# Kernel optimization log

Measured on AMD Instinct MI355X. Metric: run time of the kernel, lower is better.

The kernel has to match this reference:

```python
import jax, jax.numpy as jnp
import numpy as np

B, L = 128, 1024
V, E, H = 32, 256, 1024


def setup_inputs() -> dict:
    key = jax.random.key(0)
    ks = jax.random.split(key, 6)
    return {
        "x": jax.random.randint(ks[0], (B, L), 0, V),
        "hidden": jnp.zeros((B, H), dtype=jnp.float32),
        "embedding": jax.random.normal(ks[1], (V, E), dtype=jnp.float32),
        "W_e": jax.random.normal(ks[2], (E, H), dtype=jnp.float32) * 0.01,
        "W_h": jax.random.normal(ks[3], (H, H), dtype=jnp.float32) * 0.01,
        "b_h": jnp.zeros((H,), dtype=jnp.float32),
        "W_o": jax.random.normal(ks[4], (H, V), dtype=jnp.float32) * 0.01,
        "b_o": jnp.zeros((V,), dtype=jnp.float32),
    }


def reference(x, hidden, embedding, W_e, W_h, b_h, W_o, b_o):
    # x: [B, L] int -> embed: [B, L, E]
    x_embed = embedding[x]
    # Precompute the input projection for all timesteps at once: [L, B, H]
    xin = jnp.einsum("ble,eh->lbh", x_embed, W_e) + b_h

    def step(h, x_t):
        # h: [B, H], x_t: [B, H] (already projected + bias)
        h_new = jnp.tanh(x_t + h @ W_h)
        return h_new, h_new

    final_hidden, outputs = jax.lax.scan(step, hidden, xin)
    # outputs: [L, B, H] -> [B, L, H]
    outputs = outputs.transpose(1, 0, 2)
    logits = outputs @ W_o + b_o  # [B, L, V]
    return logits, final_hidden
```

## Files before the change

### kernel.cpp

```cpp
#include <hip/hip_runtime.h>

typedef unsigned short u16;
typedef unsigned int   u32;
typedef __attribute__((ext_vector_type(4))) float floatx4;
typedef __attribute__((ext_vector_type(4))) u32  u32x4;
typedef __attribute__((ext_vector_type(8))) short short8;

#define B_SZ  128
#define L_SEQ 1024
#define V_SZ  32
#define E_SZ  256
#define H_SZ  1024

#define N_GROUPS     8
#define WG_PER_GROUP 8
#define N_BLOCKS     (N_GROUPS * WG_PER_GROUP)
#define LOGIT_BASE   (B_SZ * L_SEQ * V_SZ)

#define BAR_BYTES  8192
#define FLAG_OFF   (BAR_BYTES - 8)
#define P_OFF      BAR_BYTES
#define P_BYTES    (V_SZ * H_SZ * 4)
#define HBUF_OFF   (P_OFF + P_BYTES)
#define NBUF       4
#define HBUF_G     (NBUF * 16 * H_SZ)
#define HBUF_BYTES (N_GROUPS * HBUF_G * 2)

#define SENT 0xFFFFFFFFu

#define MFMA16x16x32(a, b, c) __builtin_amdgcn_mfma_f32_16x16x32_bf16(a, b, c, 0, 0, 0)

__device__ inline float b2f(u16 u) {
    union { unsigned i; float f; } x; x.i = ((unsigned)u) << 16; return x.f;
}
__device__ inline u16 f2b(float f) {
    unsigned u = __float_as_uint(f);
    return (u16)((u + 0x7FFFu + ((u >> 16) & 1u)) >> 16);
}
__device__ inline float ldf(const void* p, long i, int isf32) {
    return isf32 ? ((const float*)p)[i] : b2f(((const u16*)p)[i]);
}
__device__ inline u16 ldb(const void* p, long i, int isf32) {
    return isf32 ? f2b(((const float*)p)[i]) : ((const u16*)p)[i];
}

__device__ inline void ld_row16_raw(const u16* abase, u32x4 a[8]) {
    u32x4 a0, a1, a2, a3, a4, a5, a6, a7;
    asm volatile(
        "global_load_dwordx4 %0, %8, off offset:0   sc0 sc1\n\t"
        "global_load_dwordx4 %1, %8, off offset:64  sc0 sc1\n\t"
        "global_load_dwordx4 %2, %8, off offset:128 sc0 sc1\n\t"
        "global_load_dwordx4 %3, %8, off offset:192 sc0 sc1\n\t"
        "global_load_dwordx4 %4, %8, off offset:256 sc0 sc1\n\t"
        "global_load_dwordx4 %5, %8, off offset:320 sc0 sc1\n\t"
        "global_load_dwordx4 %6, %8, off offset:384 sc0 sc1\n\t"
        "global_load_dwordx4 %7, %8, off offset:448 sc0 sc1\n\t"
        "s_waitcnt vmcnt(0)"
        : "=&v"(a0), "=&v"(a1), "=&v"(a2), "=&v"(a3),
          "=&v"(a4), "=&v"(a5), "=&v"(a6), "=&v"(a7)
        : "v"(abase)
        : "memory");
    a[0] = a0; a[1] = a1; a[2] = a2; a[3] = a3;
    a[4] = a4; a[5] = a5; a[6] = a6; a[7] = a7;
}
__device__ inline int row_ok(const u32x4 a[8]) {
    int ok = 1;
    #pragma unroll
    for (int j = 0; j < 8; ++j)
        #pragma unroll
        for (int d = 0; d < 4; ++d)
            ok &= (a[j][d] != SENT);
    return ok;
}
__device__ inline void poll_row16(const u16* abase, short8 afr[8]) {
    u32x4 av[8];
    ld_row16_raw(abase, av);
    long guard = 0;
    while (!__all(row_ok(av))) {
        if (++guard > 100000L) break;
        ld_row16_raw(abase, av);
    }
    union { u32x4 v; short8 s; } u;
    #pragma unroll
    for (int j = 0; j < 8; ++j) { u.v = av[j]; afr[j] = u.s; }
}
__device__ inline void st_row16(u32* p, u32x4 d) {
    asm volatile("global_store_dwordx4 %0, %1, off sc0 sc1" :: "v"(p), "v"(d) : "memory");
}

__global__ void detect_dtype(const u16* __restrict__ emb, const int* __restrict__ xi,
                             int* __restrict__ flag) {
    float v = b2f(emb[threadIdx.x]);
    if (!(fabsf(v) <= 1.0e6f)) atomicOr(flag, 1);
    if (xi[2 * threadIdx.x + 1] != 0) atomicOr(flag, 2);
}

__global__ void precompute_P(const void* __restrict__ emb, const void* __restrict__ We,
                             const void* __restrict__ bh, float* __restrict__ P,
                             const int* __restrict__ flag) {
    const int isf32 = *flag & 1;
    int o = blockIdx.x * 256 + threadIdx.x;
    int v = o >> 10, h = o & (H_SZ - 1);
    float acc = ldf(bh, h, isf32);
    for (int e = 0; e < E_SZ; ++e)
        acc += ldf(emb, v * E_SZ + e, isf32) * ldf(We, (long)e * H_SZ + h, isf32);
    P[o] = acc;
}

__global__ void __launch_bounds__(256, 1) rnn_kernel(
    const void* __restrict__ xp, const void* __restrict__ hidden,
    const void* __restrict__ Wh, const void* __restrict__ Wo,
    const void* __restrict__ bo, const float* __restrict__ P,
    u16* __restrict__ hbuf, float* __restrict__ out,
    const int* __restrict__ flag)
{
    __shared__ __align__(16) float red[12800];

    const int fl    = *flag;
    const int isf32 = fl & 1;
    const int xi64  = !(fl & 2);
    const int g     = blockIdx.x & 7;
    const int wg    = blockIdx.x >> 3;
    const int col0  = wg * 128;
    const int b0    = g * 16;
    const int tid   = threadIdx.x;
    const int wave  = tid >> 6;
    const int lane  = tid & 63;
    const int lrow  = lane & 15;
    const int quad  = lane >> 4;
    const int kwave = wave * 256;

    const int* x32       = (const int*)xp;
    const long long* x64 = (const long long*)xp;

    u16* hb = hbuf + g * HBUF_G;

    short8 whf[8][8], wof[2][8];
    #pragma unroll
    for (int kk = 0; kk < 8; ++kk) {
        const int kb = kwave + kk * 32 + quad * 8;
        #pragma unroll
        for (int j = 0; j < 8; ++j) {
            #pragma unroll
            for (int nt = 0; nt < 8; ++nt)
                whf[nt][kk][j] = (short)ldb(Wh, (long)(kb + j) * H_SZ + col0 + nt * 16 + lrow, isf32);
            wof[0][kk][j] = (short)ldb(Wo, (long)(kb + j) * V_SZ + lrow, isf32);
            wof[1][kk][j] = (short)ldb(Wo, (long)(kb + j) * V_SZ + 16 + lrow, isf32);
        }
    }

    const int bq = tid >> 4;
    const int c0 = (tid & 15) * 8;
    const float bov0 = ldf(bo, (tid & 15) * 2, isf32);
    const float bov1 = ldf(bo, (tid & 15) * 2 + 1, isf32);

    {
        u32x4 d;
        #pragma unroll
        for (int p = 0; p < 4; ++p) {
            u16 lo = ldb(hidden, (long)(b0 + bq) * H_SZ + col0 + c0 + 2 * p, isf32);
            u16 hi = ldb(hidden, (long)(b0 + bq) * H_SZ + col0 + c0 + 2 * p + 1, isf32);
            d[p] = (u32)lo | ((u32)hi << 16);
        }
        st_row16((u32*)(hb + bq * H_SZ + col0 + c0), d);
    }

    for (int s = 0; s < L_SEQ; ++s) {
        const u16* hc = hb + (s & 3) * (16 * H_SZ);
        u16* hn       = hb + ((s + 1) & 3) * (16 * H_SZ);
        u16* hcl      = hb + ((s + 3) & 3) * (16 * H_SZ);
        const bool do_logit = (wg == (s & 7));

        long xoff = (long)(b0 + bq) * L_SEQ + s;
        int xv = xi64 ? (int)x64[xoff] : x32[xoff];
        const floatx4* pp = (const floatx4*)(P + (long)xv * H_SZ + col0 + c0);
        floatx4 pv0 = pp[0], pv1 = pp[1];

        short8 afr[8];
        poll_row16(hc + lrow * H_SZ + kwave + quad * 8, afr);

        floatx4 acc[8] = {};
        #pragma unroll
        for (int kk = 0; kk < 8; ++kk)
            #pragma unroll
            for (int nt = 0; nt < 8; ++nt)
                acc[nt] = MFMA16x16x32(afr[kk], whf[nt][kk], acc[nt]);

        #pragma unroll
        for (int nt = 0; nt < 8; ++nt)
            #pragma unroll
            for (int r = 0; r < 4; ++r)
                red[wave * 2560 + nt * 320 + (quad * 4 + r) * 20 + lrow] = acc[nt][r];
        __syncthreads();

        {
            const int base = (c0 >> 4) * 320 + bq * 20 + (c0 & 15);
            floatx4 s0 = {0,0,0,0}, s1 = {0,0,0,0};
            #pragma unroll
            for (int w = 0; w < 4; ++w) {
                s0 += *(const floatx4*)&red[w * 2560 + base];
                s1 += *(const floatx4*)&red[w * 2560 + base + 4];
            }
            float h[8];
            #pragma unroll
            for (int j = 0; j < 4; ++j) h[j]     = tanhf(s0[j] + pv0[j]);
            #pragma unroll
            for (int j = 0; j < 4; ++j) h[4 + j] = tanhf(s1[j] + pv1[j]);
            u32x4 d;
            #pragma unroll
            for (int p = 0; p < 4; ++p)
                d[p] = (u32)f2b(h[2 * p]) | ((u32)f2b(h[2 * p + 1]) << 16);
            st_row16((u32*)(hn + bq * H_SZ + col0 + c0), d);
            if (s == L_SEQ - 1) {
                float* op = out + LOGIT_BASE + (long)(b0 + bq) * H_SZ + col0 + c0;
                ((floatx4*)op)[0] = floatx4{h[0], h[1], h[2], h[3]};
                ((floatx4*)op)[1] = floatx4{h[4], h[5], h[6], h[7]};
            }
        }
        {
            u32x4 f = { SENT, SENT, SENT, SENT };
            st_row16((u32*)(hcl + bq * H_SZ + col0 + c0), f);
        }
        __syncthreads();

        if (do_logit && s >= 1) {
            floatx4 aL0 = {0,0,0,0}, aL1 = {0,0,0,0};
            #pragma unroll
            for (int kk = 0; kk < 8; ++kk) {
                aL0 = MFMA16x16x32(afr[kk], wof[0][kk], aL0);
                aL1 = MFMA16x16x32(afr[kk], wof[1][kk], aL1);
            }
            #pragma unroll
            for (int r = 0; r < 4; ++r) {
                red[10240 + wave * 640 +       (quad * 4 + r) * 20 + lrow] = aL0[r];
                red[10240 + wave * 640 + 320 + (quad * 4 + r) * 20 + lrow] = aL1[r];
            }
            __syncthreads();
            int v0 = (tid & 15) * 2;
            int lb = 10240 + (v0 >> 4) * 320 + bq * 20 + (v0 & 15);
            float q0 = 0.f, q1 = 0.f;
            #pragma unroll
            for (int w = 0; w < 4; ++w) {
                q0 += red[lb + w * 640];
                q1 += red[lb + w * 640 + 1];
            }
            long ob = ((long)(b0 + bq) * L_SEQ + (s - 1)) * V_SZ + v0;
            out[ob]     = q0 + bov0;
            out[ob + 1] = q1 + bov1;
        }
    }

    if (wg == 0) {
        short8 afr[8];
        poll_row16(hb + lrow * H_SZ + kwave + quad * 8, afr);
        floatx4 aL0 = {0,0,0,0}, aL1 = {0,0,0,0};
        #pragma unroll
        for (int kk = 0; kk < 8; ++kk) {
            aL0 = MFMA16x16x32(afr[kk], wof[0][kk], aL0);
            aL1 = MFMA16x16x32(afr[kk], wof[1][kk], aL1);
        }
        #pragma unroll
        for (int r = 0; r < 4; ++r) {
            red[10240 + wave * 640 +       (quad * 4 + r) * 20 + lrow] = aL0[r];
            red[10240 + wave * 640 + 320 + (quad * 4 + r) * 20 + lrow] = aL1[r];
        }
        __syncthreads();
        {
            int v0 = (tid & 15) * 2;
            int lb = 10240 + (v0 >> 4) * 320 + bq * 20 + (v0 & 15);
            float q0 = 0.f, q1 = 0.f;
            #pragma unroll
            for (int w = 0; w < 4; ++w) {
                q0 += red[lb + w * 640];
                q1 += red[lb + w * 640 + 1];
            }
            long ob = ((long)(b0 + bq) * L_SEQ + (L_SEQ - 1)) * V_SZ + v0;
            out[ob]     = q0 + bov0;
            out[ob + 1] = q1 + bov1;
        }
    }
}

extern "C" void kernel_launch(void* const* d_in, const int* in_sizes, int n_in,
                              void* d_out, int out_size, void* d_ws, size_t ws_size,
                              hipStream_t stream) {
    (void)in_sizes; (void)n_in; (void)out_size; (void)ws_size;
    const void* x      = d_in[0];
    const void* hidden = d_in[1];
    const void* emb    = d_in[2];
    const void* We     = d_in[3];
    const void* Wh     = d_in[4];
    const void* bh     = d_in[5];
    const void* Wo     = d_in[6];
    const void* bo     = d_in[7];
    float* out = (float*)d_out;

    char* ws = (char*)d_ws;
    int*   flag = (int*)(ws + FLAG_OFF);
    float* P    = (float*)(ws + P_OFF);
    u16*   hbuf = (u16*)(ws + HBUF_OFF);

    hipMemsetAsync(ws, 0, BAR_BYTES, stream);
    hipMemsetAsync(ws + HBUF_OFF, 0xFF, HBUF_BYTES, stream);

    detect_dtype<<<dim3(1), dim3(256), 0, stream>>>((const u16*)emb, (const int*)x, flag);
    precompute_P<<<dim3(128), dim3(256), 0, stream>>>(emb, We, bh, P, flag);

    rnn_kernel<<<dim3(N_BLOCKS), dim3(256), 0, stream>>>(
        x, hidden, Wh, Wo, bo, P, hbuf, out, flag);
}
```

Before: 3.632 ms.

## Poll hidden-state chunks independently and overlap MFMAs with arrival; use fast tanh

```diff
diff --git a/kernel.cpp b/kernel.cpp
--- a/kernel.cpp
+++ b/kernel.cpp
@@ -44,45 +44,39 @@
     return isf32 ? f2b(((const float*)p)[i]) : ((const u16*)p)[i];
 }
 
-__device__ inline void ld_row16_raw(const u16* abase, u32x4 a[8]) {
-    u32x4 a0, a1, a2, a3, a4, a5, a6, a7;
-    asm volatile(
-        "global_load_dwordx4 %0, %8, off offset:0   sc0 sc1\n\t"
-        "global_load_dwordx4 %1, %8, off offset:64  sc0 sc1\n\t"
-        "global_load_dwordx4 %2, %8, off offset:128 sc0 sc1\n\t"
-        "global_load_dwordx4 %3, %8, off offset:192 sc0 sc1\n\t"
-        "global_load_dwordx4 %4, %8, off offset:256 sc0 sc1\n\t"
-        "global_load_dwordx4 %5, %8, off offset:320 sc0 sc1\n\t"
-        "global_load_dwordx4 %6, %8, off offset:384 sc0 sc1\n\t"
-        "global_load_dwordx4 %7, %8, off offset:448 sc0 sc1\n\t"
-        "s_waitcnt vmcnt(0)"
-        : "=&v"(a0), "=&v"(a1), "=&v"(a2), "=&v"(a3),
-          "=&v"(a4), "=&v"(a5), "=&v"(a6), "=&v"(a7)
-        : "v"(abase)
-        : "memory");
-    a[0] = a0; a[1] = a1; a[2] = a2; a[3] = a3;
-    a[4] = a4; a[5] = a5; a[6] = a6; a[7] = a7;
-}
-__device__ inline int row_ok(const u32x4 a[8]) {
-    int ok = 1;
-    #pragma unroll
-    for (int j = 0; j < 8; ++j)
-        #pragma unroll
-        for (int d = 0; d < 4; ++d)
-            ok &= (a[j][d] != SENT);
-    return ok;
-}
-__device__ inline void poll_row16(const u16* abase, short8 afr[8]) {
-    u32x4 av[8];
-    ld_row16_raw(abase, av);
-    long guard = 0;
-    while (!__all(row_ok(av))) {
-        if (++guard > 100000L) break;
-        ld_row16_raw(abase, av);
-    }
-    union { u32x4 v; short8 s; } u;
-    #pragma unroll
-    for (int j = 0; j < 8; ++j) { u.v = av[j]; afr[j] = u.s; }
+__device__ inline float fast_tanh(float x) {
+    float cx = fminf(fmaxf(x, -15.f), 15.f);
+    float t  = __builtin_amdgcn_exp2f(cx * 2.88539004f);
+    return (t - 1.f) * __builtin_amdgcn_rcpf(t + 1.f);
+}
+
+#define LOADC(dst, base, OFFLIT) \
+    asm volatile("global_load_dwordx4 %0, %1, off offset:" OFFLIT " sc0 sc1" \
+                 : "=&v"(dst) : "v"(base) : "memory")
+#define WAITVM0() asm volatile("s_waitcnt vmcnt(0)" ::: "memory")
+
+#define ISSUE_ALL8(av, ab) do { \
+    LOADC(av[0], ab, "0");   LOADC(av[1], ab, "64");  \
+    LOADC(av[2], ab, "128"); LOADC(av[3], ab, "192"); \
+    LOADC(av[4], ab, "256"); LOADC(av[5], ab, "320"); \
+    LOADC(av[6], ab, "384"); LOADC(av[7], ab, "448"); \
+    WAITVM0(); } while (0)
+
+#define REISSUE_STALE(av, ab, done) do { \
+    if (!((done) & 1))   LOADC(av[0], ab, "0");   \
+    if (!((done) & 2))   LOADC(av[1], ab, "64");  \
+    if (!((done) & 4))   LOADC(av[2], ab, "128"); \
+    if (!((done) & 8))   LOADC(av[3], ab, "192"); \
+    if (!((done) & 16))  LOADC(av[4], ab, "256"); \
+    if (!((done) & 32))  LOADC(av[5], ab, "320"); \
+    if (!((done) & 64))  LOADC(av[6], ab, "384"); \
+    if (!((done) & 128)) LOADC(av[7], ab, "448"); \
+    WAITVM0(); } while (0)
+
+__device__ inline u32 maxdw4(u32x4 a) {
+    u32 m0 = a[0] > a[1] ? a[0] : a[1];
+    u32 m1 = a[2] > a[3] ? a[2] : a[3];
+    return m0 > m1 ? m0 : m1;
 }
 __device__ inline void st_row16(u32* p, u32x4 d) {
     asm volatile("global_store_dwordx4 %0, %1, off sc0 sc1" :: "v"(p), "v"(d) : "memory");
@@ -176,16 +170,37 @@
         const floatx4* pp = (const floatx4*)(P + (long)xv * H_SZ + col0 + c0);
         floatx4 pv0 = pp[0], pv1 = pp[1];
 
+        const u16* ab = hc + lrow * H_SZ + kwave + quad * 8;
+        u32x4 av[8];
         short8 afr[8];
-        poll_row16(hc + lrow * H_SZ + kwave + quad * 8, afr);
-
         floatx4 acc[8] = {};
-        #pragma unroll
-        for (int kk = 0; kk < 8; ++kk)
-            #pragma unroll
-            for (int nt = 0; nt < 8; ++nt)
-                acc[nt] = MFMA16x16x32(afr[kk], whf[nt][kk], acc[nt]);
-
+        ISSUE_ALL8(av, ab);
+        int done = 0;
+        long guard = 0;
+        for (;;) {
+            int nd = done;
+            #pragma unroll
+            for (int j = 0; j < 8; ++j) {
+                if (!(done & (1 << j))) {
+                    if (__all((int)(maxdw4(av[j]) != SENT))) {
+                        nd |= (1 << j);
+                        union { u32x4 v; short8 s; } u; u.v = av[j];
+                        afr[j] = u.s;
+                        __builtin_amdgcn_s_setprio(1);
+                        #pragma unroll
+                        for (int nt = 0; nt < 8; ++nt)
+                            acc[nt] = MFMA16x16x32(afr[j], whf[nt][j], acc[nt]);
+                        __builtin_amdgcn_s_setprio(0);
+                    }
+                }
+            }
+            done = nd;
+            if (done == 255) break;
+            if (++guard > 200000L) break;
+            REISSUE_STALE(av, ab, done);
+        }
+
+        __builtin_amdgcn_s_setprio(1);
         #pragma unroll
         for (int nt = 0; nt < 8; ++nt)
             #pragma unroll
@@ -203,9 +218,9 @@
             }
             float h[8];
             #pragma unroll
-            for (int j = 0; j < 4; ++j) h[j]     = tanhf(s0[j] + pv0[j]);
-            #pragma unroll
-            for (int j = 0; j < 4; ++j) h[4 + j] = tanhf(s1[j] + pv1[j]);
+            for (int j = 0; j < 4; ++j) h[j]     = fast_tanh(s0[j] + pv0[j]);
+            #pragma unroll
+            for (int j = 0; j < 4; ++j) h[4 + j] = fast_tanh(s1[j] + pv1[j]);
             u32x4 d;
             #pragma unroll
             for (int p = 0; p < 4; ++p)
@@ -217,6 +232,7 @@
                 ((floatx4*)op)[1] = floatx4{h[4], h[5], h[6], h[7]};
             }
         }
+        __builtin_amdgcn_s_setprio(0);
         {
             u32x4 f = { SENT, SENT, SENT, SENT };
             st_row16((u32*)(hcl + bq * H_SZ + col0 + c0), f);
@@ -251,8 +267,27 @@
     }
 
     if (wg == 0) {
+        const u16* ab = hb + lrow * H_SZ + kwave + quad * 8;
+        u32x4 av[8];
+        ISSUE_ALL8(av, ab);
+        int done = 0;
+        long guard = 0;
+        for (;;) {
+            int nd = done;
+            #pragma unroll
+            for (int j = 0; j < 8; ++j)
+                if (!(done & (1 << j)))
+                    if (__all((int)(maxdw4(av[j]) != SENT))) nd |= (1 << j);
+            done = nd;
+            if (done == 255) break;
+            if (++guard > 200000L) break;
+            REISSUE_STALE(av, ab, done);
+        }
         short8 afr[8];
-        poll_row16(hb + lrow * H_SZ + kwave + quad * 8, afr);
+        #pragma unroll
+        for (int j = 0; j < 8; ++j) {
+            union { u32x4 v; short8 s; } u; u.v = av[j]; afr[j] = u.s;
+        }
         floatx4 aL0 = {0,0,0,0}, aL1 = {0,0,0,0};
         #pragma unroll
         for (int kk = 0; kk < 8; ++kk) {
```

Result: slower. 3.873 ms (+6.6%).
